# Optimization experiments

Hardware: AMD Instinct MI355X
Metric: run time of the kernel (lower is better)

Reference implementation:

```python
import jax, jax.numpy as jnp
import numpy as np

SIGMA_MAX = 0.3
GAMMA = 1.0
COV_SHRINK = 0.1
COV_DELTA = 1e-3
BN_EPS = 1e-5
PATCH = 3


def setup_inputs() -> dict:
    key = jax.random.key(0)
    ks = jax.random.split(key, 5)
    B, K, C, H, W = 2, 8, 64, 128, 128
    X = jax.random.normal(ks[0], (B, K, C, H, W), dtype=jnp.float32)
    w1 = jax.random.normal(ks[1], (C // 2, C), dtype=jnp.float32) * 0.1
    w2 = jax.random.normal(ks[2], (1, C // 2), dtype=jnp.float32) * 0.1
    return {
        "X": X,
        "w1": w1,
        "bn_scale": jnp.ones((C // 2,), jnp.float32),
        "bn_bias": jnp.zeros((C // 2,), jnp.float32),
        "bn_mean": jnp.zeros((C // 2,), jnp.float32),
        "bn_var": jnp.ones((C // 2,), jnp.float32),
        "w2": w2,
        "a0_raw": jax.random.normal(ks[3], (K,), dtype=jnp.float32) * 0.1,
        "sigma_raw": jax.random.normal(ks[4], (K,), dtype=jnp.float32) * 0.1,
    }


def _forward(X, w1, bn_scale, bn_bias, bn_mean, bn_var, w2, a0_raw, sigma_raw):
    B, K, C, H, W = X.shape
    # --- SensorMapGenerator: 1x1 conv -> BN (inference) -> ReLU -> 1x1 conv ---
    Xf = X.reshape(B * K, C, H, W)
    h = jnp.einsum('oc,bchw->bohw', w1, Xf)                       # [BK, C/2, H, W]
    inv_std = bn_scale / jnp.sqrt(bn_var + BN_EPS)
    h = h * inv_std[None, :, None, None] + (bn_bias - bn_mean * inv_std)[None, :, None, None]
    h = jax.nn.relu(h)
    S = jnp.einsum('oc,bchw->bohw', w2, h).reshape(B, K, H, W)    # scalar sensor maps

    # --- CovarianceEstimator: reflect pad, 3x3 patches, center, R = PP^T/N ---
    pad = PATCH // 2
    Sp = jnp.pad(S, ((0, 0), (0, 0), (pad, pad), (pad, pad)), mode='reflect')
    patches = jnp.stack(
        [Sp[:, :, i:i + H, j:j + W] for i in range(PATCH) for j in range(PATCH)],
        axis=-1)                                                  # [B, K, H, W, N]
    N = PATCH * PATCH
    patches = patches.transpose(0, 2, 3, 1, 4)                    # [B, H, W, K, N]
    pc = patches - patches.mean(axis=-1, keepdims=True)
    R = jnp.matmul(pc, pc.swapaxes(-1, -2)) / N                   # [B, H, W, K, K]

    # --- Guidance vector and uncertainty (stage mode) ---
    a0 = jax.nn.softmax(a0_raw)                                   # [K], sums to 1
    sigma = SIGMA_MAX * jax.nn.sigmoid(sigma_raw)                 # [K]

    # --- Robust diagonal-loaded Capon solve per pixel ---
    # R_reg = (1-shrink)*R + shrink*(tr R / K)*I + delta*I + gamma*diag(sigma^2)
    I = jnp.eye(K, dtype=R.dtype)
    tr = jnp.trace(R, axis1=-2, axis2=-1)                         # [B, H, W]
    load = COV_DELTA * I + GAMMA * jnp.diag(sigma * sigma)
    R_load = (1.0 - COV_SHRINK) * R + (COV_SHRINK * tr / K)[..., None, None] * I + load
    rhs = jnp.broadcast_to(a0[:, None], R_load.shape[:-2] + (K, 1))
    w_un = jnp.linalg.solve(R_load, rhs)[..., 0]                  # [B, H, W, K]
    denom = jnp.einsum('bhwk,k->bhw', w_un, a0)
    w = w_un / denom[..., None]                                   # a0^T w = 1

    # --- Weighted fusion over streams ---
    Y = jnp.einsum('bhwk,bkchw->bchw', w, X)                      # [B, C, H, W]
    return Y


def reference(X, w1, bn_scale, bn_bias, bn_mean, bn_var, w2, a0_raw, sigma_raw):
    return _forward(X, w1, bn_scale, bn_bias, bn_mean, bn_var, w2, a0_raw, sigma_raw)
```

## Files before the change

### kernel.cpp

```cpp
#include <hip/hip_runtime.h>
#include <hip/hip_bf16.h>
#include <math.h>

#define B_    2
#define K_    8
#define C_    64
#define CH_   32
#define H_    128
#define W_    128
#define HW_   16384
#define BN_EPS 1e-5f
#define SIGMA_MAX 0.3f
#define COV_SHRINK 0.1f
#define COV_DELTA 1e-3f

__global__ void prep_kernel(const float* __restrict__ w1,
                            const float* __restrict__ bn_scale,
                            const float* __restrict__ bn_bias,
                            const float* __restrict__ bn_mean,
                            const float* __restrict__ bn_var,
                            const float* __restrict__ w2,
                            const float* __restrict__ a0_raw,
                            const float* __restrict__ sigma_raw,
                            float* __restrict__ par) {
    int t = threadIdx.x;
    for (int i = t; i < CH_ * C_; i += blockDim.x) {
        int c = i >> 5;
        int o = i & 31;
        float inv = bn_scale[o] / sqrtf(bn_var[o] + BN_EPS);
        par[c * CH_ + o] = w1[o * C_ + c] * inv;
    }
    if (t < CH_) {
        float inv = bn_scale[t] / sqrtf(bn_var[t] + BN_EPS);
        par[2048 + t] = bn_bias[t] - bn_mean[t] * inv;
        par[2080 + t] = w2[t];
    }
    if (t < K_) {
        float m = -1e30f;
        for (int i = 0; i < K_; ++i) m = fmaxf(m, a0_raw[i]);
        float s = 0.f;
        for (int i = 0; i < K_; ++i) s += expf(a0_raw[i] - m);
        par[2112 + t] = expf(a0_raw[t] - m) / s;
        float sg = SIGMA_MAX / (1.f + expf(-sigma_raw[t]));
        par[2120 + t] = sg * sg;
    }
}

__global__ void __launch_bounds__(256)
stage1_kernel(const float* __restrict__ X,
              const float* __restrict__ wf,
              const float* __restrict__ beff,
              const float* __restrict__ w2,
              float* __restrict__ S) {
    int idx = blockIdx.x * blockDim.x + threadIdx.x;
    int hw = idx & (HW_ - 1);
    int bk = idx >> 14;
    const float* xp = X + (size_t)bk * (C_ * HW_) + hw;

    float acc[CH_];
#pragma unroll
    for (int o = 0; o < CH_; ++o) acc[o] = beff[o];

#pragma unroll 4
    for (int c = 0; c < C_; ++c) {
        float xv = xp[(size_t)c * HW_];
        const float* wrow = wf + c * CH_;
#pragma unroll
        for (int o = 0; o < CH_; ++o) acc[o] = fmaf(wrow[o], xv, acc[o]);
    }
    float s = 0.f;
#pragma unroll
    for (int o = 0; o < CH_; ++o) s = fmaf(w2[o], fmaxf(acc[o], 0.f), s);
    S[idx] = s;
}

__global__ void capon_kernel(const float* __restrict__ S,
                             const float* __restrict__ a0,
                             const float* __restrict__ sig2,
                             float* __restrict__ wOut) {
    int idx = blockIdx.x * blockDim.x + threadIdx.x;
    int b  = idx >> 14;
    int hw = idx & (HW_ - 1);
    int h  = hw >> 7;
    int w  = hw & (W_ - 1);

    int hm = (h == 0)      ? 1       : h - 1;
    int hp = (h == H_ - 1) ? H_ - 2  : h + 1;
    int wm = (w == 0)      ? 1       : w - 1;
    int wp = (w == W_ - 1) ? W_ - 2  : w + 1;
    int row0 = hm * W_, row1 = h * W_, row2 = hp * W_;
    int rows[3] = {row0, row1, row2};
    int cols[3] = {wm, w, wp};

    float pc[K_][9];
#pragma unroll
    for (int k = 0; k < K_; ++k) {
        const float* sp = S + (((size_t)b * K_ + k) << 14);
        float p[9];
        float m = 0.f;
#pragma unroll
        for (int i = 0; i < 3; ++i)
#pragma unroll
            for (int j = 0; j < 3; ++j) {
                float v = sp[rows[i] + cols[j]];
                p[i * 3 + j] = v;
                m += v;
            }
        m *= (1.f / 9.f);
#pragma unroll
        for (int n = 0; n < 9; ++n) pc[k][n] = p[n] - m;
    }

    float A[K_][K_];
    float tr = 0.f;
#pragma unroll
    for (int i = 0; i < K_; ++i) {
        float s = 0.f;
#pragma unroll
        for (int n = 0; n < 9; ++n) s = fmaf(pc[i][n], pc[i][n], s);
        s *= (1.f / 9.f);
        tr += s;
        A[i][i] = s;
    }
#pragma unroll
    for (int i = 0; i < K_; ++i)
#pragma unroll
        for (int j = 0; j < i; ++j) {
            float s = 0.f;
#pragma unroll
            for (int n = 0; n < 9; ++n) s = fmaf(pc[i][n], pc[j][n], s);
            A[i][j] = (1.f - COV_SHRINK) * s * (1.f / 9.f);
        }
    float dl = COV_SHRINK * tr * (1.f / (float)K_) + COV_DELTA;
#pragma unroll
    for (int i = 0; i < K_; ++i)
        A[i][i] = (1.f - COV_SHRINK) * A[i][i] + dl + sig2[i];

#pragma unroll
    for (int j = 0; j < K_; ++j) {
        float d = A[j][j];
#pragma unroll
        for (int t = 0; t < j; ++t) d = fmaf(-A[j][t], A[j][t], d);
        d = sqrtf(d);
        A[j][j] = d;
        float inv = 1.f / d;
#pragma unroll
        for (int i = j + 1; i < K_; ++i) {
            float s = A[i][j];
#pragma unroll
            for (int t = 0; t < j; ++t) s = fmaf(-A[i][t], A[j][t], s);
            A[i][j] = s * inv;
        }
    }
    float z[K_];
#pragma unroll
    for (int i = 0; i < K_; ++i) {
        float s = a0[i];
#pragma unroll
        for (int t = 0; t < i; ++t) s = fmaf(-A[i][t], z[t], s);
        z[i] = s / A[i][i];
    }
    float x[K_];
#pragma unroll
    for (int i = K_ - 1; i >= 0; --i) {
        float s = z[i];
#pragma unroll
        for (int t = i + 1; t < K_; ++t) s = fmaf(-A[t][i], x[t], s);
        x[i] = s / A[i][i];
    }
    float denom = 0.f;
#pragma unroll
    for (int k = 0; k < K_; ++k) denom = fmaf(x[k], a0[k], denom);
    float invd = 1.f / denom;

    float4 o0 = make_float4(x[0] * invd, x[1] * invd, x[2] * invd, x[3] * invd);
    float4 o1 = make_float4(x[4] * invd, x[5] * invd, x[6] * invd, x[7] * invd);
    float4* dst = (float4*)(wOut + (size_t)idx * K_);
    dst[0] = o0;
    dst[1] = o1;
}

__global__ void __launch_bounds__(256)
fuse_kernel(const float* __restrict__ X,
            const float* __restrict__ wW,
            float* __restrict__ out) {
    int idx = blockIdx.x * blockDim.x + threadIdx.x;
    int hw = idx & (HW_ - 1);
    int bc = idx >> 14;
    int b = bc >> 6;
    int c = bc & (C_ - 1);
    size_t pix = ((size_t)b << 14) + hw;

    const float4* wv4 = (const float4*)(wW + pix * K_);
    float4 wa = wv4[0];
    float4 wb = wv4[1];

    const float* xp = X + (((size_t)b * K_) * C_ + c) * HW_ + hw;
    const size_t kstride = (size_t)C_ * HW_;

    float acc;
    acc = wa.x * xp[0];
    acc = fmaf(wa.y, xp[kstride * 1], acc);
    acc = fmaf(wa.z, xp[kstride * 2], acc);
    acc = fmaf(wa.w, xp[kstride * 3], acc);
    acc = fmaf(wb.x, xp[kstride * 4], acc);
    acc = fmaf(wb.y, xp[kstride * 5], acc);
    acc = fmaf(wb.z, xp[kstride * 6], acc);
    acc = fmaf(wb.w, xp[kstride * 7], acc);
    out[idx] = acc;
}

extern "C" void kernel_launch(void* const* d_in, const int* in_sizes, int n_in,
                              void* d_out, int out_size, void* d_ws, size_t ws_size,
                              hipStream_t stream) {
    const float* X         = (const float*)d_in[0];
    const float* w1        = (const float*)d_in[1];
    const float* bn_scale  = (const float*)d_in[2];
    const float* bn_bias   = (const float*)d_in[3];
    const float* bn_mean   = (const float*)d_in[4];
    const float* bn_var    = (const float*)d_in[5];
    const float* w2        = (const float*)d_in[6];
    const float* a0_raw    = (const float*)d_in[7];
    const float* sigma_raw = (const float*)d_in[8];
    float* out = (float*)d_out;
    float* ws  = (float*)d_ws;

    float* par = ws;
    float* S   = ws + 4096;
    float* wW  = ws + 4096 + (B_ * K_ * HW_);

    prep_kernel<<<1, 256, 0, stream>>>(w1, bn_scale, bn_bias, bn_mean, bn_var,
                                       w2, a0_raw, sigma_raw, par);

    int n1 = B_ * K_ * HW_;
    stage1_kernel<<<n1 / 256, 256, 0, stream>>>(X, par, par + 2048, par + 2080, S);

    int n2 = B_ * HW_;
    capon_kernel<<<n2 / 256, 256, 0, stream>>>(S, par + 2112, par + 2120, wW);

    int n3 = B_ * C_ * HW_;
    fuse_kernel<<<n3 / 256, 256, 0, stream>>>(X, wW, out);
}
```

Baseline: 138.4 us.

## Fold parameter prep into stage1 and capon kernels, drop prep launch

Removes the single-block prep kernel. The BN folding now happens inside stage1, and the softmax and sigmoid run per thread inside the Capon kernel, which saves one launch and a serial dependency. Stage1 is also restructured to load all 64 input channels into registers first and then compute 32 dot products with split accumulators. This raises register pressure and recomputes the BN terms per thread. The fuse kernel's output now uses a nontemporal store.

New measurement: 159.3 us. 15.1% more time.

```diff
diff --git a/kernel.cpp b/kernel.cpp
--- a/kernel.cpp
+++ b/kernel.cpp
@@ -14,42 +14,13 @@
 #define COV_SHRINK 0.1f
 #define COV_DELTA 1e-3f
 
-__global__ void prep_kernel(const float* __restrict__ w1,
-                            const float* __restrict__ bn_scale,
-                            const float* __restrict__ bn_bias,
-                            const float* __restrict__ bn_mean,
-                            const float* __restrict__ bn_var,
-                            const float* __restrict__ w2,
-                            const float* __restrict__ a0_raw,
-                            const float* __restrict__ sigma_raw,
-                            float* __restrict__ par) {
-    int t = threadIdx.x;
-    for (int i = t; i < CH_ * C_; i += blockDim.x) {
-        int c = i >> 5;
-        int o = i & 31;
-        float inv = bn_scale[o] / sqrtf(bn_var[o] + BN_EPS);
-        par[c * CH_ + o] = w1[o * C_ + c] * inv;
-    }
-    if (t < CH_) {
-        float inv = bn_scale[t] / sqrtf(bn_var[t] + BN_EPS);
-        par[2048 + t] = bn_bias[t] - bn_mean[t] * inv;
-        par[2080 + t] = w2[t];
-    }
-    if (t < K_) {
-        float m = -1e30f;
-        for (int i = 0; i < K_; ++i) m = fmaxf(m, a0_raw[i]);
-        float s = 0.f;
-        for (int i = 0; i < K_; ++i) s += expf(a0_raw[i] - m);
-        par[2112 + t] = expf(a0_raw[t] - m) / s;
-        float sg = SIGMA_MAX / (1.f + expf(-sigma_raw[t]));
-        par[2120 + t] = sg * sg;
-    }
-}
-
 __global__ void __launch_bounds__(256)
 stage1_kernel(const float* __restrict__ X,
-              const float* __restrict__ wf,
-              const float* __restrict__ beff,
+              const float* __restrict__ w1,
+              const float* __restrict__ bn_scale,
+              const float* __restrict__ bn_bias,
+              const float* __restrict__ bn_mean,
+              const float* __restrict__ bn_var,
               const float* __restrict__ w2,
               float* __restrict__ S) {
     int idx = blockIdx.x * blockDim.x + threadIdx.x;
@@ -57,26 +28,33 @@
     int bk = idx >> 14;
     const float* xp = X + (size_t)bk * (C_ * HW_) + hw;
 
-    float acc[CH_];
-#pragma unroll
-    for (int o = 0; o < CH_; ++o) acc[o] = beff[o];
-
-#pragma unroll 4
-    for (int c = 0; c < C_; ++c) {
-        float xv = xp[(size_t)c * HW_];
-        const float* wrow = wf + c * CH_;
-#pragma unroll
-        for (int o = 0; o < CH_; ++o) acc[o] = fmaf(wrow[o], xv, acc[o]);
-    }
-    float s = 0.f;
-#pragma unroll
-    for (int o = 0; o < CH_; ++o) s = fmaf(w2[o], fmaxf(acc[o], 0.f), s);
-    S[idx] = s;
+    float x[C_];
+#pragma unroll
+    for (int c = 0; c < C_; ++c) x[c] = xp[(size_t)c * HW_];
+
+    float out = 0.f;
+#pragma unroll
+    for (int o = 0; o < CH_; ++o) {
+        const float* wrow = w1 + o * C_;
+        float s0 = 0.f, s1 = 0.f, s2 = 0.f, s3 = 0.f;
+#pragma unroll
+        for (int c = 0; c < C_; c += 4) {
+            s0 = fmaf(wrow[c],     x[c],     s0);
+            s1 = fmaf(wrow[c + 1], x[c + 1], s1);
+            s2 = fmaf(wrow[c + 2], x[c + 2], s2);
+            s3 = fmaf(wrow[c + 3], x[c + 3], s3);
+        }
+        float s = (s0 + s1) + (s2 + s3);
+        float inv = bn_scale[o] * rsqrtf(bn_var[o] + BN_EPS);
+        float h = fmaf(s, inv, fmaf(-bn_mean[o], inv, bn_bias[o]));
+        out = fmaf(w2[o], fmaxf(h, 0.f), out);
+    }
+    S[idx] = out;
 }
 
 __global__ void capon_kernel(const float* __restrict__ S,
-                             const float* __restrict__ a0,
-                             const float* __restrict__ sig2,
+                             const float* __restrict__ a0_raw,
+                             const float* __restrict__ sigma_raw,
                              float* __restrict__ wOut) {
     int idx = blockIdx.x * blockDim.x + threadIdx.x;
     int b  = idx >> 14;
@@ -84,12 +62,29 @@
     int h  = hw >> 7;
     int w  = hw & (W_ - 1);
 
+    float a0[K_], sig2[K_];
+    {
+        float m = -1e30f;
+#pragma unroll
+        for (int i = 0; i < K_; ++i) m = fmaxf(m, a0_raw[i]);
+        float sum = 0.f;
+#pragma unroll
+        for (int i = 0; i < K_; ++i) { a0[i] = __expf(a0_raw[i] - m); sum += a0[i]; }
+        float invs = 1.f / sum;
+#pragma unroll
+        for (int i = 0; i < K_; ++i) a0[i] *= invs;
+#pragma unroll
+        for (int i = 0; i < K_; ++i) {
+            float sg = SIGMA_MAX / (1.f + __expf(-sigma_raw[i]));
+            sig2[i] = sg * sg;
+        }
+    }
+
     int hm = (h == 0)      ? 1       : h - 1;
     int hp = (h == H_ - 1) ? H_ - 2  : h + 1;
     int wm = (w == 0)      ? 1       : w - 1;
     int wp = (w == W_ - 1) ? W_ - 2  : w + 1;
-    int row0 = hm * W_, row1 = h * W_, row2 = hp * W_;
-    int rows[3] = {row0, row1, row2};
+    int rows[3] = {hm * W_, h * W_, hp * W_};
     int cols[3] = {wm, w, wp};
 
     float pc[K_][9];
@@ -207,7 +202,7 @@
     acc = fmaf(wb.y, xp[kstride * 5], acc);
     acc = fmaf(wb.z, xp[kstride * 6], acc);
     acc = fmaf(wb.w, xp[kstride * 7], acc);
-    out[idx] = acc;
+    __builtin_nontemporal_store(acc, &out[idx]);
 }
 
 extern "C" void kernel_launch(void* const* d_in, const int* in_sizes, int n_in,
@@ -225,18 +220,15 @@
     float* out = (float*)d_out;
     float* ws  = (float*)d_ws;
 
-    float* par = ws;
-    float* S   = ws + 4096;
-    float* wW  = ws + 4096 + (B_ * K_ * HW_);
-
-    prep_kernel<<<1, 256, 0, stream>>>(w1, bn_scale, bn_bias, bn_mean, bn_var,
-                                       w2, a0_raw, sigma_raw, par);
+    float* S  = ws;
+    float* wW = ws + (B_ * K_ * HW_);
 
     int n1 = B_ * K_ * HW_;
-    stage1_kernel<<<n1 / 256, 256, 0, stream>>>(X, par, par + 2048, par + 2080, S);
+    stage1_kernel<<<n1 / 256, 256, 0, stream>>>(X, w1, bn_scale, bn_bias,
+                                                bn_mean, bn_var, w2, S);
 
     int n2 = B_ * HW_;
-    capon_kernel<<<n2 / 256, 256, 0, stream>>>(S, par + 2112, par + 2120, wW);
+    capon_kernel<<<n2 / 256, 256, 0, stream>>>(S, a0_raw, sigma_raw, wW);
 
     int n3 = B_ * C_ * HW_;
     fuse_kernel<<<n3 / 256, 256, 0, stream>>>(X, wW, out);
```
